# Performance work log

Hardware: AMD Instinct MI355X
Metric: run time of the kernel (lower is better)

## Reference

```python
import jax, jax.numpy as jnp
import numpy as np

ALPHA, GAMMA, EPS = 0.25, 2.0, 1e-8


def _safe_div(num, den):
    # tf.math.divide_no_nan semantics
    return jnp.where(den > 0, num / jnp.where(den > 0, den, 1.0), 0.0)


def giou_loss(b1, b2):
    """tfa.losses.giou_loss: boxes [ymin, xmin, ymax, xmax], broadcastable
    leading dims; returns 1 - GIoU."""
    b1_ymin, b1_xmin, b1_ymax, b1_xmax = jnp.split(b1, 4, axis=-1)
    b2_ymin, b2_xmin, b2_ymax, b2_xmax = jnp.split(b2, 4, axis=-1)
    b1_area = jnp.maximum(b1_ymax - b1_ymin, 0.0) * jnp.maximum(b1_xmax - b1_xmin, 0.0)
    b2_area = jnp.maximum(b2_ymax - b2_ymin, 0.0) * jnp.maximum(b2_xmax - b2_xmin, 0.0)
    i_ymin = jnp.maximum(b1_ymin, b2_ymin)
    i_xmin = jnp.maximum(b1_xmin, b2_xmin)
    i_ymax = jnp.minimum(b1_ymax, b2_ymax)
    i_xmax = jnp.minimum(b1_xmax, b2_xmax)
    inter = jnp.maximum(i_ymax - i_ymin, 0.0) * jnp.maximum(i_xmax - i_xmin, 0.0)
    union = b1_area + b2_area - inter
    iou = _safe_div(inter, union)
    e_ymin = jnp.minimum(b1_ymin, b2_ymin)
    e_xmin = jnp.minimum(b1_xmin, b2_xmin)
    e_ymax = jnp.maximum(b1_ymax, b2_ymax)
    e_xmax = jnp.maximum(b1_xmax, b2_xmax)
    enclose = jnp.maximum(e_ymax - e_ymin, 0.0) * jnp.maximum(e_xmax - e_xmin, 0.0)
    giou = iou - _safe_div(enclose - union, enclose)
    return (1.0 - giou)[..., 0]  # squeeze the split-kept last dim


def setup_inputs() -> dict:
    key = jax.random.key(0)
    k1, k2, k3, k4 = jax.random.split(key, 4)
    b, n, C, m = 8, 16384, 80, 100
    return {
        "cls_pred": jax.random.uniform(k1, (b, n, C), dtype=jnp.float32),
        "loc_pred": jax.random.uniform(k2, (b, n, 4), dtype=jnp.float32),
        "cls_true": jax.random.randint(k3, (b, m, C), 0, 2, dtype=jnp.int32),
        "loc_true": jax.random.uniform(k4, (b, m, 4), dtype=jnp.float32),
        "reg_mask": jnp.ones((b, m), dtype=jnp.float32),
    }


def reference(cls_pred, loc_pred, cls_true, loc_true, reg_mask):
    b, n, C = cls_pred.shape
    m = cls_true.shape[1]
    ct = (cls_true == 1).astype(jnp.float32)  # (b, m, C)

    # focal-style per-(anchor, class) cost; depends only on cls_pred, so
    # contract against the one-hot target with an einsum instead of
    # materializing a (b, m, n, C) tensor.
    p = cls_pred
    neg_cost = (1.0 - ALPHA) * p ** GAMMA * (-jnp.log(1.0 - p + EPS))
    pos_cost = ALPHA * (1.0 - p) ** GAMMA * (-jnp.log(p + EPS))
    cls_loss = jnp.einsum("bnc,bmc->bmn", pos_cost - neg_cost, ct)  # (b, m, n)

    lt = loc_true[:, :, None, :]  # (b, m, 1, 4)
    lp = loc_pred[:, None, :, :]  # (b, 1, n, 4)
    reg_loss = jnp.sum(jnp.abs(lt - lp), axis=-1)  # (b, m, n)
    giou = giou_loss(lp, lt)  # (b, m, n)

    total = 2.0 * cls_loss + 5.0 * reg_loss + 2.0 * giou
    argmin_total = jnp.argmin(total, axis=-1).astype(jnp.int32)  # (b, m)
    batch = jnp.broadcast_to(jnp.arange(b, dtype=jnp.int32)[:, None], (b, m))
    cls_id = jnp.argmax(ct, axis=-1).astype(jnp.int32)
    return jnp.stack([batch, argmin_total, cls_id], axis=-1)  # (b, m, 3)
```

## Files before the change

kernel.cpp:

```cpp
#include <hip/hip_runtime.h>

constexpr int B = 8, N = 16384, C = 80, M = 100;
constexpr int NT = 128;
constexpr int THREADS = 256;
constexpr int LDA = 104;

typedef _Float16 half8 __attribute__((ext_vector_type(8)));
typedef _Float16 half4 __attribute__((ext_vector_type(4)));
typedef float f32x4 __attribute__((ext_vector_type(4)));

constexpr size_t WS_FTAB = 0;
constexpr size_t WS_CID  = 172032;
constexpr size_t WS_PACK = 175232;

__device__ __forceinline__ unsigned ford(float f) {
    unsigned u = __float_as_uint(f);
    return (u & 0x80000000u) ? ~u : (u | 0x80000000u);
}

__device__ __forceinline__ float rcpf(float x) { return __builtin_amdgcn_rcpf(x); }

__device__ __forceinline__ float pair_total(float cls,
    float4 p, float4 t, float a1, float a2)
{
    float ih = fminf(p.z, t.z) - fmaxf(p.x, t.x);
    float iw = fminf(p.w, t.w) - fmaxf(p.y, t.y);
    float inter = fmaxf(ih, 0.f) * fmaxf(iw, 0.f);
    float uni = a1 + a2 - inter;
    float iou = (uni > 0.f) ? inter * rcpf(uni) : 0.f;
    float eh = fmaxf(p.z, t.z) - fminf(p.x, t.x);
    float ew = fmaxf(p.w, t.w) - fminf(p.y, t.y);
    float enc = fmaxf(eh, 0.f) * fmaxf(ew, 0.f);
    float ue = (enc > 0.f) ? (1.f - uni * rcpf(enc)) : 0.f;
    float one_m_giou = 1.f - iou + ue;
    float rg = fabsf(t.x - p.x) + fabsf(t.y - p.y) +
               fabsf(t.z - p.z) + fabsf(t.w - p.w);
    return 2.f * cls + 5.f * rg + 2.f * one_m_giou;
}

__global__ void prep_frag(const int* __restrict__ cls_true, uint4* __restrict__ ftab)
{
    int tid = blockIdx.x * blockDim.x + threadIdx.x;
    int f = tid >> 6, l = tid & 63;
    if (f >= B * 21) return;
    int b = f / 21, rem = f % 21, ch = rem / 7, mf = rem % 7;
    int m = mf * 16 + (l & 15);
    int c0 = ch * 32 + (l >> 4) * 8;
    unsigned w[4] = {0, 0, 0, 0};
    if (m < M) {
        const int* row = cls_true + ((size_t)b * M + m) * C;
        #pragma unroll
        for (int e = 0; e < 8; ++e) {
            int c = c0 + e;
            unsigned h = (c < C && row[c] == 1) ? 0x3C00u : 0u;
            w[e >> 1] |= h << ((e & 1) * 16);
        }
    }
    ftab[(size_t)f * 64 + l] = make_uint4(w[0], w[1], w[2], w[3]);
}

__global__ void prep_misc(const int* __restrict__ cls_true,
                          int* __restrict__ clsid,
                          unsigned long long* __restrict__ packed)
{
    int wid = (blockIdx.x * blockDim.x + threadIdx.x) >> 6;
    int l = threadIdx.x & 63;
    if (wid >= B * M) return;
    const int* row = cls_true + (size_t)wid * C;
    bool v1 = (row[l] == 1);
    bool v2 = (l < 16) ? (row[64 + l] == 1) : false;
    unsigned long long m01 = __ballot(v1);
    unsigned long long m2  = __ballot(v2);
    if (l == 0) {
        int cid = 0;
        if (m01) cid = __ffsll(m01) - 1;
        else if (m2) cid = 64 + __ffsll(m2) - 1;
        clsid[wid] = cid;
        packed[wid] = 0xFFFFFFFFFFFFFFFFull;
    }
}

__global__ __launch_bounds__(THREADS, 2)
void match_kernel(const float* __restrict__ cls_pred,
                  const float* __restrict__ loc_pred,
                  const uint4* __restrict__ ftab,
                  const float* __restrict__ loc_true,
                  unsigned long long* __restrict__ packed)
{
    __shared__ _Float16 s_hi[NT][LDA];
    __shared__ _Float16 s_lo[NT][LDA];
    __shared__ float s_lp[NT][4];
    __shared__ float s_lt[112][4];
    __shared__ unsigned long long s_red[4][112];

    const int b  = blockIdx.y;
    const int n0 = blockIdx.x * NT;
    const int t  = threadIdx.x;
    const int l  = t & 63;
    const int wv = t >> 6;

    const float4* cp4 = (const float4*)(cls_pred + ((size_t)b * N + n0) * C);
    for (int i = t; i < NT * C / 4; i += THREADS) {
        float4 v = cp4[i];
        int e = i * 4, nl = e / C, c = e % C;
        float pv[4] = { v.x, v.y, v.z, v.w };
        half4 hh, ll;
        #pragma unroll
        for (int j = 0; j < 4; ++j) {
            float p = pv[j], q = 1.0f - p;
            float pos = 0.25f * q * q * (-__logf(p + 1e-8f));
            float neg = 0.75f * p * p * (-__logf(q + 1e-8f));
            float d = pos - neg;
            _Float16 h = (_Float16)d;
            float rs = (d - (float)h) * 2048.0f;
            hh[j] = h;
            ll[j] = (_Float16)rs;
        }
        *(half4*)&s_hi[nl][c] = hh;
        *(half4*)&s_lo[nl][c] = ll;
    }
    for (int i = t; i < NT * 16 / 4; i += THREADS) {
        int nl = i >> 2, c = C + (i & 3) * 4;
        half4 z = {0, 0, 0, 0};
        *(half4*)&s_hi[nl][c] = z;
        *(half4*)&s_lo[nl][c] = z;
    }
    if (t < NT) {
        *(float4*)&s_lp[t][0] = ((const float4*)loc_pred)[(size_t)b * N + n0 + t];
    } else if (t < NT + 112) {
        int m = t - NT;
        float4 tb = (m < M) ? ((const float4*)loc_true)[(size_t)b * M + m]
                            : make_float4(0.f, 0.f, 0.f, 0.f);
        *(float4*)&s_lt[m][0] = tb;
    }
    __syncthreads();

    const int nw = wv * 32;
    f32x4 acc[2][7];
    #pragma unroll
    for (int nf = 0; nf < 2; ++nf)
        #pragma unroll
        for (int mf = 0; mf < 7; ++mf)
            acc[nf][mf] = f32x4{0.f, 0.f, 0.f, 0.f};

    const uint4* ft = ftab + (size_t)b * 21 * 64;
    const int arow = nw + (l & 15);
    const int acol = (l >> 4) * 8;

    #pragma unroll
    for (int kc = 0; kc < 3; ++kc) {
        half8 ah0 = *(const half8*)&s_hi[arow][kc * 32 + acol];
        half8 ah1 = *(const half8*)&s_hi[arow + 16][kc * 32 + acol];
        half8 al0 = *(const half8*)&s_lo[arow][kc * 32 + acol];
        half8 al1 = *(const half8*)&s_lo[arow + 16][kc * 32 + acol];
        #pragma unroll
        for (int mf = 0; mf < 7; ++mf) {
            union { uint4 u; half8 h; } b1, b2;
            b1.u = ft[((size_t)kc * 7 + mf) * 64 + l];
            b2.u = make_uint4(b1.u.x & 0x10001000u, b1.u.y & 0x10001000u,
                              b1.u.z & 0x10001000u, b1.u.w & 0x10001000u);
            acc[0][mf] = __builtin_amdgcn_mfma_f32_16x16x32_f16(ah0, b1.h, acc[0][mf], 0, 0, 0);
            acc[1][mf] = __builtin_amdgcn_mfma_f32_16x16x32_f16(ah1, b1.h, acc[1][mf], 0, 0, 0);
            acc[0][mf] = __builtin_amdgcn_mfma_f32_16x16x32_f16(al0, b2.h, acc[0][mf], 0, 0, 0);
            acc[1][mf] = __builtin_amdgcn_mfma_f32_16x16x32_f16(al1, b2.h, acc[1][mf], 0, 0, 0);
        }
    }

    float4 bx[2][4];
    float a1[2][4];
    #pragma unroll
    for (int nf = 0; nf < 2; ++nf)
        #pragma unroll
        for (int r = 0; r < 4; ++r) {
            int row = nw + nf * 16 + (l >> 4) * 4 + r;
            float4 v = *(const float4*)&s_lp[row][0];
            bx[nf][r] = v;
            a1[nf][r] = fmaxf(v.z - v.x, 0.f) * fmaxf(v.w - v.y, 0.f);
        }

    #pragma unroll
    for (int mf = 0; mf < 7; ++mf) {
        float4 tb = *(const float4*)&s_lt[mf * 16 + (l & 15)][0];
        float a2 = fmaxf(tb.z - tb.x, 0.f) * fmaxf(tb.w - tb.y, 0.f);
        unsigned long long cand = 0xFFFFFFFFFFFFFFFFull;
        #pragma unroll
        for (int nf = 0; nf < 2; ++nf)
            #pragma unroll
            for (int r = 0; r < 4; ++r) {
                float tot = pair_total(acc[nf][mf][r], bx[nf][r], tb, a1[nf][r], a2);
                int n = n0 + nw + nf * 16 + (l >> 4) * 4 + r;
                unsigned long long key =
                    ((unsigned long long)ford(tot) << 32) | (unsigned)n;
                cand = (key < cand) ? key : cand;
            }
        #pragma unroll
        for (int off = 16; off <= 32; off <<= 1) {
            unsigned long long o = __shfl_xor(cand, off, 64);
            if (o < cand) cand = o;
        }
        if (l < 16) s_red[wv][mf * 16 + l] = cand;
    }
    __syncthreads();

    if (t < 112) {
        unsigned long long v0 = s_red[0][t], v1 = s_red[1][t];
        unsigned long long v2 = s_red[2][t], v3 = s_red[3][t];
        unsigned long long a = v0 < v1 ? v0 : v1;
        unsigned long long c2 = v2 < v3 ? v2 : v3;
        a = a < c2 ? a : c2;
        if (t < M) atomicMin(&packed[(size_t)b * M + t], a);
    }
}

__global__ void out_kernel(const unsigned long long* __restrict__ packed,
                           const int* __restrict__ clsid,
                           int* __restrict__ out)
{
    int idx = blockIdx.x * blockDim.x + threadIdx.x;
    if (idx >= B * M) return;
    int b = idx / M;
    out[idx * 3 + 0] = b;
    out[idx * 3 + 1] = (int)(unsigned)(packed[idx] & 0xFFFFFFFFull);
    out[idx * 3 + 2] = clsid[idx];
}

extern "C" void kernel_launch(void* const* d_in, const int* in_sizes, int n_in,
                              void* d_out, int out_size, void* d_ws, size_t ws_size,
                              hipStream_t stream)
{
    const float* cls_pred = (const float*)d_in[0];
    const float* loc_pred = (const float*)d_in[1];
    const int*   cls_true = (const int*)d_in[2];
    const float* loc_true = (const float*)d_in[3];

    char* ws = (char*)d_ws;
    uint4* ftab = (uint4*)(ws + WS_FTAB);
    int*   clsid = (int*)(ws + WS_CID);
    unsigned long long* packed = (unsigned long long*)(ws + WS_PACK);

    int* out = (int*)d_out;

    prep_frag<<<(B * 21 * 64 + 255) / 256, 256, 0, stream>>>(cls_true, ftab);
    prep_misc<<<(B * M * 64 + 255) / 256, 256, 0, stream>>>(cls_true, clsid, packed);

    dim3 grid(N / NT, B);
    match_kernel<<<grid, THREADS, 0, stream>>>(
        cls_pred, loc_pred, ftab, loc_true, packed);

    out_kernel<<<(B * M + 255) / 256, 256, 0, stream>>>(packed, clsid, out);
}
```

Measured before the change: 55.01 us.

## Halve anchor tile, merge prep kernels, and rescale total cost

Reduces the anchor tile from 128 to 64 so each wave handles one 16-row MFMA fragment, doubling the grid and raising launch bounds to 4 blocks per CU for more occupancy and less per-thread register pressure. Merges the two preprocessing kernels into one launch to cut launch overhead. Divides the cost expression by 2 and uses an fma, which keeps the argmin unchanged while saving multiplies. In exchange, the one-hot fragment table is reloaded by twice as many blocks and more atomics hit the output slots.

```diff
diff --git a/kernel.cpp b/kernel.cpp
--- a/kernel.cpp
+++ b/kernel.cpp
@@ -1,7 +1,7 @@
 #include <hip/hip_runtime.h>
 
 constexpr int B = 8, N = 16384, C = 80, M = 100;
-constexpr int NT = 128;
+constexpr int NT = 64;
 constexpr int THREADS = 256;
 constexpr int LDA = 104;
 
@@ -32,55 +32,51 @@
     float ew = fmaxf(p.w, t.w) - fminf(p.y, t.y);
     float enc = fmaxf(eh, 0.f) * fmaxf(ew, 0.f);
     float ue = (enc > 0.f) ? (1.f - uni * rcpf(enc)) : 0.f;
-    float one_m_giou = 1.f - iou + ue;
     float rg = fabsf(t.x - p.x) + fabsf(t.y - p.y) +
                fabsf(t.z - p.z) + fabsf(t.w - p.w);
-    return 2.f * cls + 5.f * rg + 2.f * one_m_giou;
-}
-
-__global__ void prep_frag(const int* __restrict__ cls_true, uint4* __restrict__ ftab)
-{
-    int tid = blockIdx.x * blockDim.x + threadIdx.x;
-    int f = tid >> 6, l = tid & 63;
-    if (f >= B * 21) return;
-    int b = f / 21, rem = f % 21, ch = rem / 7, mf = rem % 7;
-    int m = mf * 16 + (l & 15);
-    int c0 = ch * 32 + (l >> 4) * 8;
-    unsigned w[4] = {0, 0, 0, 0};
-    if (m < M) {
-        const int* row = cls_true + ((size_t)b * M + m) * C;
-        #pragma unroll
-        for (int e = 0; e < 8; ++e) {
-            int c = c0 + e;
-            unsigned h = (c < C && row[c] == 1) ? 0x3C00u : 0u;
-            w[e >> 1] |= h << ((e & 1) * 16);
-        }
-    }
-    ftab[(size_t)f * 64 + l] = make_uint4(w[0], w[1], w[2], w[3]);
-}
-
-__global__ void prep_misc(const int* __restrict__ cls_true,
-                          int* __restrict__ clsid,
-                          unsigned long long* __restrict__ packed)
+    return fmaf(2.5f, rg, cls) + (1.f - iou + ue);
+}
+
+__global__ void prep_kernel(const int* __restrict__ cls_true,
+                            uint4* __restrict__ ftab,
+                            int* __restrict__ clsid,
+                            unsigned long long* __restrict__ packed)
 {
     int wid = (blockIdx.x * blockDim.x + threadIdx.x) >> 6;
     int l = threadIdx.x & 63;
-    if (wid >= B * M) return;
-    const int* row = cls_true + (size_t)wid * C;
-    bool v1 = (row[l] == 1);
-    bool v2 = (l < 16) ? (row[64 + l] == 1) : false;
-    unsigned long long m01 = __ballot(v1);
-    unsigned long long m2  = __ballot(v2);
-    if (l == 0) {
-        int cid = 0;
-        if (m01) cid = __ffsll(m01) - 1;
-        else if (m2) cid = 64 + __ffsll(m2) - 1;
-        clsid[wid] = cid;
-        packed[wid] = 0xFFFFFFFFFFFFFFFFull;
-    }
-}
-
-__global__ __launch_bounds__(THREADS, 2)
+    if (wid < B * 21) {
+        int b = wid / 21, rem = wid % 21, ch = rem / 7, mf = rem % 7;
+        int m = mf * 16 + (l & 15);
+        int c0 = ch * 32 + (l >> 4) * 8;
+        unsigned w[4] = {0, 0, 0, 0};
+        if (m < M) {
+            const int* row = cls_true + ((size_t)b * M + m) * C;
+            #pragma unroll
+            for (int e = 0; e < 8; ++e) {
+                int c = c0 + e;
+                unsigned h = (c < C && row[c] == 1) ? 0x3C00u : 0u;
+                w[e >> 1] |= h << ((e & 1) * 16);
+            }
+        }
+        ftab[(size_t)wid * 64 + l] = make_uint4(w[0], w[1], w[2], w[3]);
+    } else if (wid < B * 21 + B * M) {
+        int id = wid - B * 21;
+        const int* row = cls_true + (size_t)id * C;
+        bool v1 = (row[l] == 1);
+        bool v2 = (l < 16) ? (row[64 + l] == 1) : false;
+        unsigned long long m01 = __ballot(v1);
+        unsigned long long m2  = __ballot(v2);
+        if (l == 0) {
+            int cid = 0;
+            if (m01) cid = __ffsll(m01) - 1;
+            else if (m2) cid = 64 + __ffsll(m2) - 1;
+            clsid[id] = cid;
+            packed[id] = 0xFFFFFFFFFFFFFFFFull;
+        }
+    }
+}
+
+__global__ __launch_bounds__(THREADS, 4)
 void match_kernel(const float* __restrict__ cls_pred,
                   const float* __restrict__ loc_pred,
                   const uint4* __restrict__ ftab,
@@ -119,11 +115,14 @@
         *(half4*)&s_hi[nl][c] = hh;
         *(half4*)&s_lo[nl][c] = ll;
     }
-    for (int i = t; i < NT * 16 / 4; i += THREADS) {
-        int nl = i >> 2, c = C + (i & 3) * 4;
-        half4 z = {0, 0, 0, 0};
-        *(half4*)&s_hi[nl][c] = z;
-        *(half4*)&s_lo[nl][c] = z;
+    {
+        int i = t;
+        if (i < NT * 4) {
+            int nl = i >> 2, c = C + (i & 3) * 4;
+            half4 z = {0, 0, 0, 0};
+            *(half4*)&s_hi[nl][c] = z;
+            *(half4*)&s_lo[nl][c] = z;
+        }
     }
     if (t < NT) {
         *(float4*)&s_lp[t][0] = ((const float4*)loc_pred)[(size_t)b * N + n0 + t];
@@ -135,13 +134,10 @@
     }
     __syncthreads();
 
-    const int nw = wv * 32;
-    f32x4 acc[2][7];
-    #pragma unroll
-    for (int nf = 0; nf < 2; ++nf)
-        #pragma unroll
-        for (int mf = 0; mf < 7; ++mf)
-            acc[nf][mf] = f32x4{0.f, 0.f, 0.f, 0.f};
+    const int nw = wv * 16;
+    f32x4 acc[7];
+    #pragma unroll
+    for (int mf = 0; mf < 7; ++mf) acc[mf] = f32x4{0.f, 0.f, 0.f, 0.f};
 
     const uint4* ft = ftab + (size_t)b * 21 * 64;
     const int arow = nw + (l & 15);
@@ -149,34 +145,28 @@
 
     #pragma unroll
     for (int kc = 0; kc < 3; ++kc) {
-        half8 ah0 = *(const half8*)&s_hi[arow][kc * 32 + acol];
-        half8 ah1 = *(const half8*)&s_hi[arow + 16][kc * 32 + acol];
-        half8 al0 = *(const half8*)&s_lo[arow][kc * 32 + acol];
-        half8 al1 = *(const half8*)&s_lo[arow + 16][kc * 32 + acol];
+        half8 ah = *(const half8*)&s_hi[arow][kc * 32 + acol];
+        half8 al = *(const half8*)&s_lo[arow][kc * 32 + acol];
         #pragma unroll
         for (int mf = 0; mf < 7; ++mf) {
             union { uint4 u; half8 h; } b1, b2;
             b1.u = ft[((size_t)kc * 7 + mf) * 64 + l];
             b2.u = make_uint4(b1.u.x & 0x10001000u, b1.u.y & 0x10001000u,
                               b1.u.z & 0x10001000u, b1.u.w & 0x10001000u);
-            acc[0][mf] = __builtin_amdgcn_mfma_f32_16x16x32_f16(ah0, b1.h, acc[0][mf], 0, 0, 0);
-            acc[1][mf] = __builtin_amdgcn_mfma_f32_16x16x32_f16(ah1, b1.h, acc[1][mf], 0, 0, 0);
-            acc[0][mf] = __builtin_amdgcn_mfma_f32_16x16x32_f16(al0, b2.h, acc[0][mf], 0, 0, 0);
-            acc[1][mf] = __builtin_amdgcn_mfma_f32_16x16x32_f16(al1, b2.h, acc[1][mf], 0, 0, 0);
-        }
-    }
-
-    float4 bx[2][4];
-    float a1[2][4];
-    #pragma unroll
-    for (int nf = 0; nf < 2; ++nf)
-        #pragma unroll
-        for (int r = 0; r < 4; ++r) {
-            int row = nw + nf * 16 + (l >> 4) * 4 + r;
-            float4 v = *(const float4*)&s_lp[row][0];
-            bx[nf][r] = v;
-            a1[nf][r] = fmaxf(v.z - v.x, 0.f) * fmaxf(v.w - v.y, 0.f);
-        }
+            acc[mf] = __builtin_amdgcn_mfma_f32_16x16x32_f16(ah, b1.h, acc[mf], 0, 0, 0);
+            acc[mf] = __builtin_amdgcn_mfma_f32_16x16x32_f16(al, b2.h, acc[mf], 0, 0, 0);
+        }
+    }
+
+    float4 bx[4];
+    float a1[4];
+    #pragma unroll
+    for (int r = 0; r < 4; ++r) {
+        int row = nw + (l >> 4) * 4 + r;
+        float4 v = *(const float4*)&s_lp[row][0];
+        bx[r] = v;
+        a1[r] = fmaxf(v.z - v.x, 0.f) * fmaxf(v.w - v.y, 0.f);
+    }
 
     #pragma unroll
     for (int mf = 0; mf < 7; ++mf) {
@@ -184,15 +174,13 @@
         float a2 = fmaxf(tb.z - tb.x, 0.f) * fmaxf(tb.w - tb.y, 0.f);
         unsigned long long cand = 0xFFFFFFFFFFFFFFFFull;
         #pragma unroll
-        for (int nf = 0; nf < 2; ++nf)
-            #pragma unroll
-            for (int r = 0; r < 4; ++r) {
-                float tot = pair_total(acc[nf][mf][r], bx[nf][r], tb, a1[nf][r], a2);
-                int n = n0 + nw + nf * 16 + (l >> 4) * 4 + r;
-                unsigned long long key =
-                    ((unsigned long long)ford(tot) << 32) | (unsigned)n;
-                cand = (key < cand) ? key : cand;
-            }
+        for (int r = 0; r < 4; ++r) {
+            float tot = pair_total(acc[mf][r], bx[r], tb, a1[r], a2);
+            int n = n0 + nw + (l >> 4) * 4 + r;
+            unsigned long long key =
+                ((unsigned long long)ford(tot) << 32) | (unsigned)n;
+            cand = (key < cand) ? key : cand;
+        }
         #pragma unroll
         for (int off = 16; off <= 32; off <<= 1) {
             unsigned long long o = __shfl_xor(cand, off, 64);
@@ -240,8 +228,9 @@
 
     int* out = (int*)d_out;
 
-    prep_frag<<<(B * 21 * 64 + 255) / 256, 256, 0, stream>>>(cls_true, ftab);
-    prep_misc<<<(B * M * 64 + 255) / 256, 256, 0, stream>>>(cls_true, clsid, packed);
+    int prep_waves = B * 21 + B * M;
+    prep_kernel<<<(prep_waves * 64 + 255) / 256, 256, 0, stream>>>(
+        cls_true, ftab, clsid, packed);
 
     dim3 grid(N / NT, B);
     match_kernel<<<grid, THREADS, 0, stream>>>(
```

Result: slower. 57.74 us (+5.0%).
